# Optimization experiments

Measured on AMD Instinct MI355X. Metric: run time of the kernel, lower is better.

## Reference

```python
import jax, jax.numpy as jnp
import numpy as np

N_GRAPHS = 64

def setup_inputs() -> dict:
    key = jax.random.key(0)
    ks = jax.random.split(key, 8)
    N, E, H = 50000, 600000, 128
    x = jax.random.normal(ks[0], (N, 2), dtype=jnp.float32)
    edge_index = jax.random.randint(ks[1], (2, E), 0, N, dtype=jnp.int64)
    batch = jnp.sort(jax.random.randint(ks[2], (N,), 0, N_GRAPHS, dtype=jnp.int64))
    s = 0.1  # keep tanh out of saturation
    return {
        'x': x,
        'edge_index': edge_index,
        'batch': batch,
        'W1': jax.random.normal(ks[3], (2, H), dtype=jnp.float32) * s,
        'b1': jnp.zeros((H,), jnp.float32),
        'W2': jax.random.normal(ks[4], (H, H), dtype=jnp.float32) * s,
        'b2': jnp.zeros((H,), jnp.float32),
        'W3': jax.random.normal(ks[5], (H, H), dtype=jnp.float32) * s,
        'b3': jnp.zeros((H,), jnp.float32),
        'Wo': jax.random.normal(ks[6], (2 * H, 41), dtype=jnp.float32) * s,
        'bo': jnp.zeros((41,), jnp.float32),
    }

def reference(x, edge_index, batch, W1, b1, W2, b2, W3, b3, Wo, bo):
    N = x.shape[0]
    src, dst = edge_index[0], edge_index[1]
    # GCN symmetric normalization with self loops: deg = in-degree + 1
    ones_e = jnp.ones(src.shape[0], dtype=x.dtype)
    deg = jax.ops.segment_sum(ones_e, dst, num_segments=N) + 1.0
    dinv = jax.lax.rsqrt(deg)                       # [N]
    edge_norm = (dinv[src] * dinv[dst])[:, None]    # [E,1]
    self_norm = (dinv * dinv)[:, None]              # [N,1]

    def gcn(h, W, b):
        h = h @ W                                   # [N,H] transform first
        agg = jax.ops.segment_sum(h[src] * edge_norm, dst, num_segments=N)
        return agg + h * self_norm + b

    h = jnp.tanh(gcn(x, W1, b1))
    h = jnp.tanh(gcn(h, W2, b2))
    h = jnp.tanh(gcn(h, W3, b3))

    # global max pool + global mean pool over graphs
    cnt = jax.ops.segment_sum(jnp.ones(N, dtype=h.dtype), batch, num_segments=N_GRAPHS)
    mx = jax.ops.segment_max(h, batch, num_segments=N_GRAPHS)
    mx = jnp.where(cnt[:, None] > 0, mx, 0.0)
    mean = jax.ops.segment_sum(h, batch, num_segments=N_GRAPHS) / jnp.maximum(cnt, 1.0)[:, None]
    pooled = jnp.concatenate([mx, mean], axis=1)    # [G, 2H]
    return jnp.tanh(pooled @ Wo + bo)               # [G, 41]
```

## Files before the change

### kernel.cpp

```cpp
#include <hip/hip_runtime.h>
#include <math.h>

#define NGRAPH 64
#define POOL_CHUNKS 32
#define SCAN_BLK 1024

typedef short short8 __attribute__((ext_vector_type(8)));
typedef float floatx4 __attribute__((ext_vector_type(4)));

__device__ inline unsigned pack_bf16x2(float a, float b) {
    unsigned ua = __float_as_uint(a);
    unsigned ub = __float_as_uint(b);
    ua = (ua + 0x7fffu + ((ua >> 16) & 1u)) >> 16;
    ub = (ub + 0x7fffu + ((ub >> 16) & 1u)) >> 16;
    return ua | (ub << 16);
}
__device__ inline unsigned short bf16_1(float a) {
    unsigned ua = __float_as_uint(a);
    return (unsigned short)((ua + 0x7fffu + ((ua >> 16) & 1u)) >> 16);
}


__global__ void count_kernel(const int* __restrict__ dst, int E, int* __restrict__ cnt) {
    int e = blockIdx.x * blockDim.x + threadIdx.x;
    if (e < E) atomicAdd(&cnt[dst[e]], 1);
}

__global__ __launch_bounds__(SCAN_BLK) void scan_phase1(const int* __restrict__ cnt,
                                                        const float* __restrict__ x,
                                                        int* __restrict__ row_ptr,
                                                        int* __restrict__ bsum,
                                                        float* __restrict__ dinv,
                                                        float2* __restrict__ y, int N) {
    __shared__ int sm[SCAN_BLK];
    int i = blockIdx.x * SCAN_BLK + threadIdx.x;
    int v = (i < N) ? cnt[i] : 0;
    if (i < N) {
        float dv = rsqrtf((float)v + 1.0f);
        dinv[i] = dv;
        float2 xv = ((const float2*)x)[i];
        y[i] = make_float2(xv.x * dv, xv.y * dv);
    }
    sm[threadIdx.x] = v;
    __syncthreads();
    for (int off = 1; off < SCAN_BLK; off <<= 1) {
        int t = (threadIdx.x >= (unsigned)off) ? sm[threadIdx.x - off] : 0;
        __syncthreads();
        sm[threadIdx.x] += t;
        __syncthreads();
    }
    if (i < N) row_ptr[i] = sm[threadIdx.x] - v;
    if (threadIdx.x == SCAN_BLK - 1) bsum[blockIdx.x] = sm[SCAN_BLK - 1];
}

__global__ __launch_bounds__(SCAN_BLK) void scan_phase2(int* __restrict__ bsum, int nb,
                                                        const int* __restrict__ batch, int N,
                                                        int* __restrict__ goff) {
    if (threadIdx.x <= NGRAPH) {
        int g = threadIdx.x;
        int lo = 0, hi = N;
        while (lo < hi) {
            int mid = (lo + hi) >> 1;
            if (batch[mid] < g) lo = mid + 1; else hi = mid;
        }
        goff[g] = lo;
    }
    __shared__ int sm[SCAN_BLK];
    int v = (threadIdx.x < (unsigned)nb) ? bsum[threadIdx.x] : 0;
    sm[threadIdx.x] = v;
    __syncthreads();
    for (int off = 1; off < SCAN_BLK; off <<= 1) {
        int t = (threadIdx.x >= (unsigned)off) ? sm[threadIdx.x - off] : 0;
        __syncthreads();
        sm[threadIdx.x] += t;
        __syncthreads();
    }
    if (threadIdx.x < (unsigned)nb) bsum[threadIdx.x] = sm[threadIdx.x] - v;
}

__global__ __launch_bounds__(SCAN_BLK) void scan_phase3(int* __restrict__ row_ptr,
                                                        const int* __restrict__ bsum,
                                                        int N, int E) {
    int i = blockIdx.x * SCAN_BLK + threadIdx.x;
    if (i < N) row_ptr[i] += bsum[blockIdx.x];
    if (i == 0) row_ptr[N] = E;
}

__global__ void fill_kernel(const int* __restrict__ src, const int* __restrict__ dst, int E,
                            const int* __restrict__ row_ptr, int* __restrict__ cnt,
                            int* __restrict__ col) {
    int e = blockIdx.x * blockDim.x + threadIdx.x;
    if (e < E) {
        int d = dst[e];
        int p = row_ptr[d] + atomicSub(&cnt[d], 1) - 1;
        col[p] = src[e];
    }
}


__global__ __launch_bounds__(256) void packWt(const float* __restrict__ W2,
                                              const float* __restrict__ W3,
                                              unsigned* __restrict__ Wt2,
                                              unsigned* __restrict__ Wt3) {
    int b = blockIdx.x;
    const float* W = (b < 16) ? W2 : W3;
    unsigned* Wt = (b < 16) ? Wt2 : Wt3;
    b &= 15;
    int bk = b & 3, bn = b >> 2;
    __shared__ float s[32][33];
    int tx = threadIdx.x & 31, ty = threadIdx.x >> 5;
#pragma unroll
    for (int r = 0; r < 4; ++r)
        s[r * 8 + ty][tx] = W[(bk * 32 + r * 8 + ty) * 128 + bn * 32 + tx];
    __syncthreads();
    int t16 = threadIdx.x & 15, tn = threadIdx.x >> 4;
#pragma unroll
    for (int pass = 0; pass < 2; ++pass) {
        int nl = pass * 16 + tn;
        unsigned pk = pack_bf16x2(s[2 * t16][nl], s[2 * t16 + 1][nl]);
        Wt[(bn * 32 + nl) * 64 + bk * 16 + t16] = pk;
    }
}


__global__ __launch_bounds__(256) void agg_x_kernel(const float2* __restrict__ y,
                                                    const int* __restrict__ row_ptr,
                                                    const int* __restrict__ col,
                                                    const float* __restrict__ dinv,
                                                    float2* __restrict__ z, int N) {
    int v = blockIdx.x * blockDim.x + threadIdx.x;
    if (v >= N) return;
    int s = row_ptr[v], e = row_ptr[v + 1];
    float2 a0 = y[v];
    float2 a1 = make_float2(0.f, 0.f);
    float2 a2 = make_float2(0.f, 0.f);
    float2 a3 = make_float2(0.f, 0.f);
    int j = s;
    for (; j + 4 <= e; j += 4) {
        int u0 = col[j], u1 = col[j + 1], u2 = col[j + 2], u3 = col[j + 3];
        float2 v0 = y[u0], v1 = y[u1], v2 = y[u2], v3 = y[u3];
        a0.x += v0.x; a0.y += v0.y;
        a1.x += v1.x; a1.y += v1.y;
        a2.x += v2.x; a2.y += v2.y;
        a3.x += v3.x; a3.y += v3.y;
    }
    for (; j < e; ++j) {
        float2 vv = y[col[j]];
        a0.x += vv.x; a0.y += vv.y;
    }
    float dv = dinv[v];
    z[v] = make_float2(dv * (a0.x + a1.x + a2.x + a3.x),
                       dv * (a0.y + a1.y + a2.y + a3.y));
}

__global__ __launch_bounds__(256) void transform1(const float2* __restrict__ z,
                                                  const float* __restrict__ W1,
                                                  const float* __restrict__ b1,
                                                  unsigned short* __restrict__ h, int N) {
    int tid = blockIdx.x * blockDim.x + threadIdx.x;
    int row = tid >> 5;
    if (row >= N) return;
    int q = tid & 31;
    float2 zv = z[row];
    const float4* W4 = (const float4*)W1;
    float4 w0 = W4[q];
    float4 w1 = W4[32 + q];
    float4 b = ((const float4*)b1)[q];
    float ox = tanhf(fmaf(zv.x, w0.x, fmaf(zv.y, w1.x, b.x)));
    float oy = tanhf(fmaf(zv.x, w0.y, fmaf(zv.y, w1.y, b.y)));
    float oz = tanhf(fmaf(zv.x, w0.z, fmaf(zv.y, w1.z, b.z)));
    float ow = tanhf(fmaf(zv.x, w0.w, fmaf(zv.y, w1.w, b.w)));
    uint2 pk;
    pk.x = pack_bf16x2(ox, oy);
    pk.y = pack_bf16x2(oz, ow);
    ((uint2*)h)[row * 32 + q] = pk;
}


__global__ __launch_bounds__(256) void gemm_mfma(const unsigned short* __restrict__ A,
                                                 const unsigned* __restrict__ Wt,
                                                 const float* __restrict__ dinv,
                                                 unsigned short* __restrict__ t, int N) {
    __shared__ unsigned sW[128 * 68];
    const uint4* Wt4 = (const uint4*)Wt;
    for (int i = threadIdx.x; i < 2048; i += 256) {
        int n = i >> 4, c = i & 15;
        *(uint4*)&sW[n * 68 + c * 4] = Wt4[i];
    }
    __syncthreads();
    int w = threadIdx.x >> 6;
    int l = threadIdx.x & 63;
    int lm = l & 15;
    int q4 = l >> 4;
    int k8 = q4 * 8;

    floatx4 acc[2][8];
#pragma unroll
    for (int i = 0; i < 2; ++i)
#pragma unroll
        for (int j = 0; j < 8; ++j) acc[i][j] = (floatx4){0.f, 0.f, 0.f, 0.f};

    int rowbase = blockIdx.x * 128 + w * 32;
#pragma unroll
    for (int ks = 0; ks < 4; ++ks) {
        int k0 = ks * 32 + k8;
        short8 a[2];
#pragma unroll
        for (int mt = 0; mt < 2; ++mt) {
            int r = min(rowbase + mt * 16 + lm, N - 1);
            a[mt] = *(const short8*)(A + (size_t)r * 128 + k0);
        }
#pragma unroll
        for (int nt = 0; nt < 8; ++nt) {
            short8 b = *(const short8*)&sW[(nt * 16 + lm) * 68 + ks * 16 + q4 * 4];
#pragma unroll
            for (int mt = 0; mt < 2; ++mt)
                acc[mt][nt] = __builtin_amdgcn_mfma_f32_16x16x32_bf16(a[mt], b, acc[mt][nt], 0, 0, 0);
        }
    }

#pragma unroll
    for (int mt = 0; mt < 2; ++mt) {
#pragma unroll
        for (int reg = 0; reg < 4; ++reg) {
            int gr = rowbase + mt * 16 + q4 * 4 + reg;
            if (gr >= N) continue;
            float dv = dinv[gr];
#pragma unroll
            for (int nt = 0; nt < 8; ++nt) {
                int c = nt * 16 + lm;
                t[(size_t)gr * 128 + c] = bf16_1(acc[mt][nt][reg] * dv);
            }
        }
    }
}


template <bool BF16OUT>
__global__ __launch_bounds__(256) void agg_kernel(const unsigned short* __restrict__ t,
                                                  const int* __restrict__ row_ptr,
                                                  const int* __restrict__ col,
                                                  const float* __restrict__ dinv,
                                                  const float* __restrict__ bias,
                                                  float* __restrict__ outF,
                                                  unsigned short* __restrict__ outB, int N) {
    int wave = threadIdx.x >> 6;
    int lane = threadIdx.x & 63;
    int sub  = lane >> 4;
    int q    = lane & 15;
    int node = blockIdx.x * 16 + wave * 4 + sub;
    if (node >= N) return;
    int s = row_ptr[node];
    int deg = row_ptr[node + 1] - s;
    const uint4* t4 = (const uint4*)t;
    float acc[4][8];
    {
        uint4 sd = t4[(size_t)node * 16 + q];
        acc[0][0] = __uint_as_float(sd.x << 16);
        acc[0][1] = __uint_as_float(sd.x & 0xffff0000u);
        acc[0][2] = __uint_as_float(sd.y << 16);
        acc[0][3] = __uint_as_float(sd.y & 0xffff0000u);
        acc[0][4] = __uint_as_float(sd.z << 16);
        acc[0][5] = __uint_as_float(sd.z & 0xffff0000u);
        acc[0][6] = __uint_as_float(sd.w << 16);
        acc[0][7] = __uint_as_float(sd.w & 0xffff0000u);
    }
#pragma unroll
    for (int i = 1; i < 4; ++i)
#pragma unroll
        for (int k = 0; k < 8; ++k) acc[i][k] = 0.f;
    int j = 0;
    for (; j + 4 <= deg; j += 4) {
        int u[4];
#pragma unroll
        for (int i = 0; i < 4; ++i) u[i] = col[s + j + i];
        uint4 v[4];
#pragma unroll
        for (int i = 0; i < 4; ++i) v[i] = t4[(size_t)u[i] * 16 + q];
#pragma unroll
        for (int i = 0; i < 4; ++i) {
            acc[i][0] += __uint_as_float(v[i].x << 16);
            acc[i][1] += __uint_as_float(v[i].x & 0xffff0000u);
            acc[i][2] += __uint_as_float(v[i].y << 16);
            acc[i][3] += __uint_as_float(v[i].y & 0xffff0000u);
            acc[i][4] += __uint_as_float(v[i].z << 16);
            acc[i][5] += __uint_as_float(v[i].z & 0xffff0000u);
            acc[i][6] += __uint_as_float(v[i].w << 16);
            acc[i][7] += __uint_as_float(v[i].w & 0xffff0000u);
        }
    }
    for (; j < deg; ++j) {
        uint4 v = t4[(size_t)col[s + j] * 16 + q];
        acc[0][0] += __uint_as_float(v.x << 16);
        acc[0][1] += __uint_as_float(v.x & 0xffff0000u);
        acc[0][2] += __uint_as_float(v.y << 16);
        acc[0][3] += __uint_as_float(v.y & 0xffff0000u);
        acc[0][4] += __uint_as_float(v.z << 16);
        acc[0][5] += __uint_as_float(v.z & 0xffff0000u);
        acc[0][6] += __uint_as_float(v.w << 16);
        acc[0][7] += __uint_as_float(v.w & 0xffff0000u);
    }
#pragma unroll
    for (int i = 1; i < 4; ++i)
#pragma unroll
        for (int k = 0; k < 8; ++k) acc[0][k] += acc[i][k];
    float dv = dinv[node];
    float4 b0 = ((const float4*)bias)[2 * q];
    float4 b1 = ((const float4*)bias)[2 * q + 1];
    float o[8];
    o[0] = tanhf(fmaf(dv, acc[0][0], b0.x));
    o[1] = tanhf(fmaf(dv, acc[0][1], b0.y));
    o[2] = tanhf(fmaf(dv, acc[0][2], b0.z));
    o[3] = tanhf(fmaf(dv, acc[0][3], b0.w));
    o[4] = tanhf(fmaf(dv, acc[0][4], b1.x));
    o[5] = tanhf(fmaf(dv, acc[0][5], b1.y));
    o[6] = tanhf(fmaf(dv, acc[0][6], b1.z));
    o[7] = tanhf(fmaf(dv, acc[0][7], b1.w));
    if (BF16OUT) {
        uint4 pk;
        pk.x = pack_bf16x2(o[0], o[1]);
        pk.y = pack_bf16x2(o[2], o[3]);
        pk.z = pack_bf16x2(o[4], o[5]);
        pk.w = pack_bf16x2(o[6], o[7]);
        ((uint4*)outB)[(size_t)node * 16 + q] = pk;
    } else {
        ((float4*)outF)[(size_t)node * 32 + 2 * q]     = make_float4(o[0], o[1], o[2], o[3]);
        ((float4*)outF)[(size_t)node * 32 + 2 * q + 1] = make_float4(o[4], o[5], o[6], o[7]);
    }
}


__global__ __launch_bounds__(128) void pool_partial(const float* __restrict__ h,
                                                    const int* __restrict__ goff,
                                                    float* __restrict__ part) {
    int g = blockIdx.x;
    int c = blockIdx.y;
    int j = threadIdx.x;
    int s = goff[g], e = goff[g + 1];
    int cnt = e - s;
    int per = (cnt + POOL_CHUNKS - 1) / POOL_CHUNKS;
    int ps = s + c * per;
    int pe = min(ps + per, e);
    float mx = -3.402823466e+38f, sm = 0.f;
    for (int n = ps; n < pe; ++n) {
        float v = h[(size_t)n * 128 + j];
        mx = fmaxf(mx, v);
        sm += v;
    }
    float* dst = part + ((size_t)g * POOL_CHUNKS + c) * 256;
    dst[j] = mx;
    dst[128 + j] = sm;
}

__global__ __launch_bounds__(128) void pool_final(const float* __restrict__ part,
                                                  const int* __restrict__ goff,
                                                  const float* __restrict__ Wo,
                                                  const float* __restrict__ bo,
                                                  float* __restrict__ out) {
    __shared__ float p[256];
    int g = blockIdx.x;
    int j = threadIdx.x;
    float mx = -3.402823466e+38f, sm = 0.f;
    const float* base = part + (size_t)g * POOL_CHUNKS * 256;
#pragma unroll 4
    for (int c = 0; c < POOL_CHUNKS; ++c) {
        mx = fmaxf(mx, base[c * 256 + j]);
        sm += base[c * 256 + 128 + j];
    }
    int cnt = goff[g + 1] - goff[g];
    p[j] = (cnt > 0) ? mx : 0.f;
    p[128 + j] = sm / fmaxf((float)cnt, 1.f);
    __syncthreads();
    if (j < 41) {
        float acc = bo[j];
        for (int k = 0; k < 256; ++k) acc = fmaf(p[k], Wo[k * 41 + j], acc);
        out[g * 41 + j] = tanhf(acc);
    }
}


extern "C" void kernel_launch(void* const* d_in, const int* in_sizes, int n_in,
                              void* d_out, int out_size, void* d_ws, size_t ws_size,
                              hipStream_t stream) {
    const float* x   = (const float*)d_in[0];
    const int*   ei  = (const int*)d_in[1];
    const int* batch = (const int*)d_in[2];
    const float* W1  = (const float*)d_in[3];
    const float* b1  = (const float*)d_in[4];
    const float* W2  = (const float*)d_in[5];
    const float* b2  = (const float*)d_in[6];
    const float* W3  = (const float*)d_in[7];
    const float* b3  = (const float*)d_in[8];
    const float* Wo  = (const float*)d_in[9];
    const float* bo  = (const float*)d_in[10];
    float* outp = (float*)d_out;

    int N = in_sizes[2];
    int E = in_sizes[1] / 2;
    const int* src = ei;
    const int* dst = ei + E;

    char* p = (char*)d_ws;
    auto alloc = [&](size_t bytes) -> char* {
        char* q = p;
        p += (bytes + 255) & ~(size_t)255;
        return q;
    };
    unsigned short* t  = (unsigned short*)alloc((size_t)N * 128 * 2);
    unsigned short* hb = (unsigned short*)alloc((size_t)N * 128 * 2);
    float* h3     = (float*)alloc((size_t)N * 128 * 4);
    float* dinv   = (float*)alloc((size_t)N * 4);
    int*   cnt    = (int*)alloc((size_t)N * 4);
    int*   rowp   = (int*)alloc((size_t)(N + 1) * 4);
    int*   col    = (int*)alloc((size_t)E * 4);
    int*   goff   = (int*)alloc(65 * 4);
    float* part   = (float*)alloc((size_t)NGRAPH * POOL_CHUNKS * 256 * 4);
    float2* y     = (float2*)alloc((size_t)N * 8);
    float2* z     = (float2*)alloc((size_t)N * 8);
    unsigned* Wt2 = (unsigned*)alloc(128 * 64 * 4);
    unsigned* Wt3 = (unsigned*)alloc(128 * 64 * 4);
    int nscan = (N + SCAN_BLK - 1) / SCAN_BLK;
    int*   bsum   = (int*)alloc((size_t)nscan * 4);

    hipMemsetAsync(cnt, 0, (size_t)N * 4, stream);

    packWt<<<32, 256, 0, stream>>>(W2, W3, Wt2, Wt3);
    count_kernel<<<(E + 255) / 256, 256, 0, stream>>>(dst, E, cnt);
    scan_phase1<<<nscan, SCAN_BLK, 0, stream>>>(cnt, x, rowp, bsum, dinv, y, N);
    scan_phase2<<<1, SCAN_BLK, 0, stream>>>(bsum, nscan, batch, N, goff);
    scan_phase3<<<nscan, SCAN_BLK, 0, stream>>>(rowp, bsum, N, E);
    fill_kernel<<<(E + 255) / 256, 256, 0, stream>>>(src, dst, E, rowp, cnt, col);

    agg_x_kernel<<<(N + 255) / 256, 256, 0, stream>>>(y, rowp, col, dinv, z, N);
    transform1<<<((size_t)N * 32 + 255) / 256, 256, 0, stream>>>(z, W1, b1, hb, N);
    gemm_mfma<<<(N + 127) / 128, 256, 0, stream>>>(hb, Wt2, dinv, t, N);
    agg_kernel<true><<<(N + 15) / 16, 256, 0, stream>>>(t, rowp, col, dinv, b2, nullptr, hb, N);
    gemm_mfma<<<(N + 127) / 128, 256, 0, stream>>>(hb, Wt3, dinv, t, N);
    agg_kernel<false><<<(N + 15) / 16, 256, 0, stream>>>(t, rowp, col, dinv, b3, h3, nullptr, N);

    dim3 pgrid(NGRAPH, POOL_CHUNKS);
    pool_partial<<<pgrid, 128, 0, stream>>>(h3, goff, part);
    pool_final<<<NGRAPH, 128, 0, stream>>>(part, goff, Wo, bo, outp);
}
```

Baseline: 273.0 us.

## Fuse small kernels, remap aggregation to one node per wave, store final h as bf16

Merges the weight packing and degree count into one launch, and fuses the first-layer aggregation with its 2->128 transform, dropping the intermediate z buffer. The aggregation kernel now assigns one node per wave, with four lane groups splitting that node's neighbours and combining through shuffles, instead of four nodes per wave each walking its own neighbour list. The last layer's output is written as bf16, not fp32, which halves pooling read traffic at some cost in precision. These changes aim to cut launch overhead and memory traffic and to improve load balance across uneven degrees.

```diff
diff --git a/kernel.cpp b/kernel.cpp
--- a/kernel.cpp
+++ b/kernel.cpp
@@ -19,12 +19,38 @@
     unsigned ua = __float_as_uint(a);
     return (unsigned short)((ua + 0x7fffu + ((ua >> 16) & 1u)) >> 16);
 }
-
-
-__global__ void count_kernel(const int* __restrict__ dst, int E, int* __restrict__ cnt) {
-    int e = blockIdx.x * blockDim.x + threadIdx.x;
-    if (e < E) atomicAdd(&cnt[dst[e]], 1);
-}
+__device__ inline float bf16lo(unsigned u) { return __uint_as_float(u << 16); }
+__device__ inline float bf16hi(unsigned u) { return __uint_as_float(u & 0xffff0000u); }
+
+
+__global__ void pack_count(const int* __restrict__ dst, int E, int* __restrict__ cnt,
+                           const float* __restrict__ W2, const float* __restrict__ W3,
+                           unsigned* __restrict__ Wt2, unsigned* __restrict__ Wt3) {
+    if (blockIdx.x < 32) {
+        int b = blockIdx.x;
+        const float* W = (b < 16) ? W2 : W3;
+        unsigned* Wt = (b < 16) ? Wt2 : Wt3;
+        b &= 15;
+        int bk = b & 3, bn = b >> 2;
+        __shared__ float s[32][33];
+        int tx = threadIdx.x & 31, ty = threadIdx.x >> 5;
+#pragma unroll
+        for (int r = 0; r < 4; ++r)
+            s[r * 8 + ty][tx] = W[(bk * 32 + r * 8 + ty) * 128 + bn * 32 + tx];
+        __syncthreads();
+        int t16 = threadIdx.x & 15, tn = threadIdx.x >> 4;
+#pragma unroll
+        for (int pass = 0; pass < 2; ++pass) {
+            int nl = pass * 16 + tn;
+            unsigned pk = pack_bf16x2(s[2 * t16][nl], s[2 * t16 + 1][nl]);
+            Wt[(bn * 32 + nl) * 64 + bk * 16 + t16] = pk;
+        }
+    } else {
+        int e = (blockIdx.x - 32) * blockDim.x + threadIdx.x;
+        if (e < E) atomicAdd(&cnt[dst[e]], 1);
+    }
+}
+
 
 __global__ __launch_bounds__(SCAN_BLK) void scan_phase1(const int* __restrict__ cnt,
                                                         const float* __restrict__ x,
@@ -98,82 +124,67 @@
 }
 
 
-__global__ __launch_bounds__(256) void packWt(const float* __restrict__ W2,
-                                              const float* __restrict__ W3,
-                                              unsigned* __restrict__ Wt2,
-                                              unsigned* __restrict__ Wt3) {
-    int b = blockIdx.x;
-    const float* W = (b < 16) ? W2 : W3;
-    unsigned* Wt = (b < 16) ? Wt2 : Wt3;
-    b &= 15;
-    int bk = b & 3, bn = b >> 2;
-    __shared__ float s[32][33];
-    int tx = threadIdx.x & 31, ty = threadIdx.x >> 5;
-#pragma unroll
-    for (int r = 0; r < 4; ++r)
-        s[r * 8 + ty][tx] = W[(bk * 32 + r * 8 + ty) * 128 + bn * 32 + tx];
+__global__ __launch_bounds__(256) void agg_x_t1(const float2* __restrict__ y,
+                                                const int* __restrict__ row_ptr,
+                                                const int* __restrict__ col,
+                                                const float* __restrict__ dinv,
+                                                const float* __restrict__ W1,
+                                                const float* __restrict__ b1,
+                                                unsigned short* __restrict__ h, int N) {
+    __shared__ float4 sW[64];
+    __shared__ float4 sb[32];
+    __shared__ float2 zs[256];
+    if (threadIdx.x < 64) sW[threadIdx.x] = ((const float4*)W1)[threadIdx.x];
+    if (threadIdx.x < 32) sb[threadIdx.x] = ((const float4*)b1)[threadIdx.x];
+
+    int v = blockIdx.x * 256 + threadIdx.x;
+    float2 zv = make_float2(0.f, 0.f);
+    if (v < N) {
+        int s = row_ptr[v], e = row_ptr[v + 1];
+        float2 a0 = y[v];
+        float2 a1 = make_float2(0.f, 0.f);
+        float2 a2 = make_float2(0.f, 0.f);
+        float2 a3 = make_float2(0.f, 0.f);
+        int j = s;
+        for (; j + 4 <= e; j += 4) {
+            int u0 = col[j], u1 = col[j + 1], u2 = col[j + 2], u3 = col[j + 3];
+            float2 v0 = y[u0], v1 = y[u1], v2 = y[u2], v3 = y[u3];
+            a0.x += v0.x; a0.y += v0.y;
+            a1.x += v1.x; a1.y += v1.y;
+            a2.x += v2.x; a2.y += v2.y;
+            a3.x += v3.x; a3.y += v3.y;
+        }
+        for (; j < e; ++j) {
+            float2 vv = y[col[j]];
+            a0.x += vv.x; a0.y += vv.y;
+        }
+        float dv = dinv[v];
+        zv = make_float2(dv * (a0.x + a1.x + a2.x + a3.x),
+                         dv * (a0.y + a1.y + a2.y + a3.y));
+    }
+    zs[threadIdx.x] = zv;
     __syncthreads();
-    int t16 = threadIdx.x & 15, tn = threadIdx.x >> 4;
-#pragma unroll
-    for (int pass = 0; pass < 2; ++pass) {
-        int nl = pass * 16 + tn;
-        unsigned pk = pack_bf16x2(s[2 * t16][nl], s[2 * t16 + 1][nl]);
-        Wt[(bn * 32 + nl) * 64 + bk * 16 + t16] = pk;
-    }
-}
-
-
-__global__ __launch_bounds__(256) void agg_x_kernel(const float2* __restrict__ y,
-                                                    const int* __restrict__ row_ptr,
-                                                    const int* __restrict__ col,
-                                                    const float* __restrict__ dinv,
-                                                    float2* __restrict__ z, int N) {
-    int v = blockIdx.x * blockDim.x + threadIdx.x;
-    if (v >= N) return;
-    int s = row_ptr[v], e = row_ptr[v + 1];
-    float2 a0 = y[v];
-    float2 a1 = make_float2(0.f, 0.f);
-    float2 a2 = make_float2(0.f, 0.f);
-    float2 a3 = make_float2(0.f, 0.f);
-    int j = s;
-    for (; j + 4 <= e; j += 4) {
-        int u0 = col[j], u1 = col[j + 1], u2 = col[j + 2], u3 = col[j + 3];
-        float2 v0 = y[u0], v1 = y[u1], v2 = y[u2], v3 = y[u3];
-        a0.x += v0.x; a0.y += v0.y;
-        a1.x += v1.x; a1.y += v1.y;
-        a2.x += v2.x; a2.y += v2.y;
-        a3.x += v3.x; a3.y += v3.y;
-    }
-    for (; j < e; ++j) {
-        float2 vv = y[col[j]];
-        a0.x += vv.x; a0.y += vv.y;
-    }
-    float dv = dinv[v];
-    z[v] = make_float2(dv * (a0.x + a1.x + a2.x + a3.x),
-                       dv * (a0.y + a1.y + a2.y + a3.y));
-}
-
-__global__ __launch_bounds__(256) void transform1(const float2* __restrict__ z,
-                                                  const float* __restrict__ W1,
-                                                  const float* __restrict__ b1,
-                                                  unsigned short* __restrict__ h, int N) {
-    int tid = blockIdx.x * blockDim.x + threadIdx.x;
-    int row = tid >> 5;
-    if (row >= N) return;
-    int q = tid & 31;
-    float2 zv = z[row];
-    const float4* W4 = (const float4*)W1;
-    float4 w0 = W4[q];
-    float4 w1 = W4[32 + q];
-    float4 b = ((const float4*)b1)[q];
-    float ox = tanhf(fmaf(zv.x, w0.x, fmaf(zv.y, w1.x, b.x)));
-    float oy = tanhf(fmaf(zv.x, w0.y, fmaf(zv.y, w1.y, b.y)));
-    float oz = tanhf(fmaf(zv.x, w0.z, fmaf(zv.y, w1.z, b.z)));
-    float ow = tanhf(fmaf(zv.x, w0.w, fmaf(zv.y, w1.w, b.w)));
-    uint2 pk;
-    pk.x = pack_bf16x2(ox, oy);
-    pk.y = pack_bf16x2(oz, ow);
-    ((uint2*)h)[row * 32 + q] = pk;
+
+    int q = threadIdx.x & 31;
+    int rsub = threadIdx.x >> 5;
+    float4 w0 = sW[q];
+    float4 w1 = sW[32 + q];
+    float4 b = sb[q];
+#pragma unroll 4
+    for (int pass = 0; pass < 32; ++pass) {
+        int local = pass * 8 + rsub;
+        int row = blockIdx.x * 256 + local;
+        if (row >= N) break;
+        float2 z = zs[local];
+        float ox = tanhf(fmaf(z.x, w0.x, fmaf(z.y, w1.x, b.x)));
+        float oy = tanhf(fmaf(z.x, w0.y, fmaf(z.y, w1.y, b.y)));
+        float oz = tanhf(fmaf(z.x, w0.z, fmaf(z.y, w1.z, b.z)));
+        float ow = tanhf(fmaf(z.x, w0.w, fmaf(z.y, w1.w, b.w)));
+        uint2 pk;
+        pk.x = pack_bf16x2(ox, oy);
+        pk.y = pack_bf16x2(oz, ow);
+        ((uint2*)h)[(size_t)row * 32 + q] = pk;
+    }
 }
 
 
@@ -236,101 +247,79 @@
 }
 
 
-template <bool BF16OUT>
 __global__ __launch_bounds__(256) void agg_kernel(const unsigned short* __restrict__ t,
                                                   const int* __restrict__ row_ptr,
                                                   const int* __restrict__ col,
                                                   const float* __restrict__ dinv,
                                                   const float* __restrict__ bias,
-                                                  float* __restrict__ outF,
-                                                  unsigned short* __restrict__ outB, int N) {
+                                                  unsigned short* __restrict__ out, int N) {
     int wave = threadIdx.x >> 6;
     int lane = threadIdx.x & 63;
-    int sub  = lane >> 4;
-    int q    = lane & 15;
-    int node = blockIdx.x * 16 + wave * 4 + sub;
+    int i = lane >> 4;
+    int q = lane & 15;
+    int node = blockIdx.x * 4 + wave;
     if (node >= N) return;
     int s = row_ptr[node];
     int deg = row_ptr[node + 1] - s;
     const uint4* t4 = (const uint4*)t;
-    float acc[4][8];
-    {
-        uint4 sd = t4[(size_t)node * 16 + q];
-        acc[0][0] = __uint_as_float(sd.x << 16);
-        acc[0][1] = __uint_as_float(sd.x & 0xffff0000u);
-        acc[0][2] = __uint_as_float(sd.y << 16);
-        acc[0][3] = __uint_as_float(sd.y & 0xffff0000u);
-        acc[0][4] = __uint_as_float(sd.z << 16);
-        acc[0][5] = __uint_as_float(sd.z & 0xffff0000u);
-        acc[0][6] = __uint_as_float(sd.w << 16);
-        acc[0][7] = __uint_as_float(sd.w & 0xffff0000u);
-    }
-#pragma unroll
-    for (int i = 1; i < 4; ++i)
-#pragma unroll
-        for (int k = 0; k < 8; ++k) acc[i][k] = 0.f;
+
+    float a0[8], a1[8];
+#pragma unroll
+    for (int k = 0; k < 8; ++k) { a0[k] = 0.f; a1[k] = 0.f; }
+    if (i == 0) {
+        uint4 v = t4[(size_t)node * 16 + q];
+        a0[0] = bf16lo(v.x); a0[1] = bf16hi(v.x);
+        a0[2] = bf16lo(v.y); a0[3] = bf16hi(v.y);
+        a0[4] = bf16lo(v.z); a0[5] = bf16hi(v.z);
+        a0[6] = bf16lo(v.w); a0[7] = bf16hi(v.w);
+    }
     int j = 0;
-    for (; j + 4 <= deg; j += 4) {
-        int u[4];
-#pragma unroll
-        for (int i = 0; i < 4; ++i) u[i] = col[s + j + i];
-        uint4 v[4];
-#pragma unroll
-        for (int i = 0; i < 4; ++i) v[i] = t4[(size_t)u[i] * 16 + q];
-#pragma unroll
-        for (int i = 0; i < 4; ++i) {
-            acc[i][0] += __uint_as_float(v[i].x << 16);
-            acc[i][1] += __uint_as_float(v[i].x & 0xffff0000u);
-            acc[i][2] += __uint_as_float(v[i].y << 16);
-            acc[i][3] += __uint_as_float(v[i].y & 0xffff0000u);
-            acc[i][4] += __uint_as_float(v[i].z << 16);
-            acc[i][5] += __uint_as_float(v[i].z & 0xffff0000u);
-            acc[i][6] += __uint_as_float(v[i].w << 16);
-            acc[i][7] += __uint_as_float(v[i].w & 0xffff0000u);
-        }
-    }
-    for (; j < deg; ++j) {
-        uint4 v = t4[(size_t)col[s + j] * 16 + q];
-        acc[0][0] += __uint_as_float(v.x << 16);
-        acc[0][1] += __uint_as_float(v.x & 0xffff0000u);
-        acc[0][2] += __uint_as_float(v.y << 16);
-        acc[0][3] += __uint_as_float(v.y & 0xffff0000u);
-        acc[0][4] += __uint_as_float(v.z << 16);
-        acc[0][5] += __uint_as_float(v.z & 0xffff0000u);
-        acc[0][6] += __uint_as_float(v.w << 16);
-        acc[0][7] += __uint_as_float(v.w & 0xffff0000u);
-    }
-#pragma unroll
-    for (int i = 1; i < 4; ++i)
-#pragma unroll
-        for (int k = 0; k < 8; ++k) acc[0][k] += acc[i][k];
-    float dv = dinv[node];
-    float4 b0 = ((const float4*)bias)[2 * q];
-    float4 b1 = ((const float4*)bias)[2 * q + 1];
-    float o[8];
-    o[0] = tanhf(fmaf(dv, acc[0][0], b0.x));
-    o[1] = tanhf(fmaf(dv, acc[0][1], b0.y));
-    o[2] = tanhf(fmaf(dv, acc[0][2], b0.z));
-    o[3] = tanhf(fmaf(dv, acc[0][3], b0.w));
-    o[4] = tanhf(fmaf(dv, acc[0][4], b1.x));
-    o[5] = tanhf(fmaf(dv, acc[0][5], b1.y));
-    o[6] = tanhf(fmaf(dv, acc[0][6], b1.z));
-    o[7] = tanhf(fmaf(dv, acc[0][7], b1.w));
-    if (BF16OUT) {
+    for (; j + 8 <= deg; j += 8) {
+        int u0 = col[s + j + i];
+        int u1 = col[s + j + 4 + i];
+        uint4 v0 = t4[(size_t)u0 * 16 + q];
+        uint4 v1 = t4[(size_t)u1 * 16 + q];
+        a0[0] += bf16lo(v0.x); a0[1] += bf16hi(v0.x);
+        a0[2] += bf16lo(v0.y); a0[3] += bf16hi(v0.y);
+        a0[4] += bf16lo(v0.z); a0[5] += bf16hi(v0.z);
+        a0[6] += bf16lo(v0.w); a0[7] += bf16hi(v0.w);
+        a1[0] += bf16lo(v1.x); a1[1] += bf16hi(v1.x);
+        a1[2] += bf16lo(v1.y); a1[3] += bf16hi(v1.y);
+        a1[4] += bf16lo(v1.z); a1[5] += bf16hi(v1.z);
+        a1[6] += bf16lo(v1.w); a1[7] += bf16hi(v1.w);
+    }
+    for (; j < deg; j += 4) {
+        if (j + i < deg) {
+            int u = col[s + j + i];
+            uint4 v = t4[(size_t)u * 16 + q];
+            a0[0] += bf16lo(v.x); a0[1] += bf16hi(v.x);
+            a0[2] += bf16lo(v.y); a0[3] += bf16hi(v.y);
+            a0[4] += bf16lo(v.z); a0[5] += bf16hi(v.z);
+            a0[6] += bf16lo(v.w); a0[7] += bf16hi(v.w);
+        }
+    }
+#pragma unroll
+    for (int k = 0; k < 8; ++k) {
+        float v = a0[k] + a1[k];
+        v += __shfl_xor(v, 16, 64);
+        v += __shfl_xor(v, 32, 64);
+        a0[k] = v;
+    }
+    if (i == 0) {
+        float dv = dinv[node];
+        float4 b0 = ((const float4*)bias)[2 * q];
+        float4 b1 = ((const float4*)bias)[2 * q + 1];
         uint4 pk;
-        pk.x = pack_bf16x2(o[0], o[1]);
-        pk.y = pack_bf16x2(o[2], o[3]);
-        pk.z = pack_bf16x2(o[4], o[5]);
-        pk.w = pack_bf16x2(o[6], o[7]);
-        ((uint4*)outB)[(size_t)node * 16 + q] = pk;
-    } else {
-        ((float4*)outF)[(size_t)node * 32 + 2 * q]     = make_float4(o[0], o[1], o[2], o[3]);
-        ((float4*)outF)[(size_t)node * 32 + 2 * q + 1] = make_float4(o[4], o[5], o[6], o[7]);
-    }
-}
-
-
-__global__ __launch_bounds__(128) void pool_partial(const float* __restrict__ h,
+        pk.x = pack_bf16x2(tanhf(fmaf(dv, a0[0], b0.x)), tanhf(fmaf(dv, a0[1], b0.y)));
+        pk.y = pack_bf16x2(tanhf(fmaf(dv, a0[2], b0.z)), tanhf(fmaf(dv, a0[3], b0.w)));
+        pk.z = pack_bf16x2(tanhf(fmaf(dv, a0[4], b1.x)), tanhf(fmaf(dv, a0[5], b1.y)));
+        pk.w = pack_bf16x2(tanhf(fmaf(dv, a0[6], b1.z)), tanhf(fmaf(dv, a0[7], b1.w)));
+        ((uint4*)out)[(size_t)node * 16 + q] = pk;
+    }
+}
+
+
+__global__ __launch_bounds__(128) void pool_partial(const unsigned short* __restrict__ h,
                                                     const int* __restrict__ goff,
                                                     float* __restrict__ part) {
     int g = blockIdx.x;
@@ -343,7 +332,7 @@
     int pe = min(ps + per, e);
     float mx = -3.402823466e+38f, sm = 0.f;
     for (int n = ps; n < pe; ++n) {
-        float v = h[(size_t)n * 128 + j];
+        float v = __uint_as_float(((unsigned)h[(size_t)n * 128 + j]) << 16);
         mx = fmaxf(mx, v);
         sm += v;
     }
@@ -406,9 +395,9 @@
         p += (bytes + 255) & ~(size_t)255;
         return q;
     };
-    unsigned short* t  = (unsigned short*)alloc((size_t)N * 128 * 2);
-    unsigned short* hb = (unsigned short*)alloc((size_t)N * 128 * 2);
-    float* h3     = (float*)alloc((size_t)N * 128 * 4);
+    unsigned short* t   = (unsigned short*)alloc((size_t)N * 128 * 2);
+    unsigned short* hb  = (unsigned short*)alloc((size_t)N * 128 * 2);
+    unsigned short* h3b = (unsigned short*)alloc((size_t)N * 128 * 2);
     float* dinv   = (float*)alloc((size_t)N * 4);
     int*   cnt    = (int*)alloc((size_t)N * 4);
     int*   rowp   = (int*)alloc((size_t)(N + 1) * 4);
@@ -416,7 +405,6 @@
     int*   goff   = (int*)alloc(65 * 4);
     float* part   = (float*)alloc((size_t)NGRAPH * POOL_CHUNKS * 256 * 4);
     float2* y     = (float2*)alloc((size_t)N * 8);
-    float2* z     = (float2*)alloc((size_t)N * 8);
     unsigned* Wt2 = (unsigned*)alloc(128 * 64 * 4);
     unsigned* Wt3 = (unsigned*)alloc(128 * 64 * 4);
     int nscan = (N + SCAN_BLK - 1) / SCAN_BLK;
@@ -424,21 +412,19 @@
 
     hipMemsetAsync(cnt, 0, (size_t)N * 4, stream);
 
-    packWt<<<32, 256, 0, stream>>>(W2, W3, Wt2, Wt3);
-    count_kernel<<<(E + 255) / 256, 256, 0, stream>>>(dst, E, cnt);
+    pack_count<<<32 + (E + 255) / 256, 256, 0, stream>>>(dst, E, cnt, W2, W3, Wt2, Wt3);
     scan_phase1<<<nscan, SCAN_BLK, 0, stream>>>(cnt, x, rowp, bsum, dinv, y, N);
     scan_phase2<<<1, SCAN_BLK, 0, stream>>>(bsum, nscan, batch, N, goff);
     scan_phase3<<<nscan, SCAN_BLK, 0, stream>>>(rowp, bsum, N, E);
     fill_kernel<<<(E + 255) / 256, 256, 0, stream>>>(src, dst, E, rowp, cnt, col);
 
-    agg_x_kernel<<<(N + 255) / 256, 256, 0, stream>>>(y, rowp, col, dinv, z, N);
-    transform1<<<((size_t)N * 32 + 255) / 256, 256, 0, stream>>>(z, W1, b1, hb, N);
+    agg_x_t1<<<(N + 255) / 256, 256, 0, stream>>>(y, rowp, col, dinv, W1, b1, hb, N);
     gemm_mfma<<<(N + 127) / 128, 256, 0, stream>>>(hb, Wt2, dinv, t, N);
-    agg_kernel<true><<<(N + 15) / 16, 256, 0, stream>>>(t, rowp, col, dinv, b2, nullptr, hb, N);
+    agg_kernel<<<(N + 3) / 4, 256, 0, stream>>>(t, rowp, col, dinv, b2, hb, N);
     gemm_mfma<<<(N + 127) / 128, 256, 0, stream>>>(hb, Wt3, dinv, t, N);
-    agg_kernel<false><<<(N + 15) / 16, 256, 0, stream>>>(t, rowp, col, dinv, b3, h3, nullptr, N);
+    agg_kernel<<<(N + 3) / 4, 256, 0, stream>>>(t, rowp, col, dinv, b3, h3b, N);
 
     dim3 pgrid(NGRAPH, POOL_CHUNKS);
-    pool_partial<<<pgrid, 128, 0, stream>>>(h3, goff, part);
+    pool_partial<<<pgrid, 128, 0, stream>>>(h3b, goff, part);
     pool_final<<<NGRAPH, 128, 0, stream>>>(part, goff, Wo, bo, outp);
 }
```

Result: no change. 272.2 us (-0.3%).
